# Optimization experiments

Measured on AMD Instinct MI355X. Metric: run time of the kernel, lower is better.

Reference implementation:

```python
import jax, jax.numpy as jnp
import numpy as np

N, C, H, W = 128, 3, 256, 256
MAXNORM = 5.371920351148152
MAX_SQ = 16  # static bound for data-dependent squaring loop
PADE_B = [6.476475253248e+16, 3.238237626624e+16, 7771770303897600.0,
          1187353796428800.0, 129060195264000.0, 10559470521600.0,
          670442572800.0, 33522128640.0, 1323241920.0, 40840800.0,
          960960.0, 16380.0, 182.0, 1.0]


def pade13(A):
    b = PADE_B
    I = jnp.eye(A.shape[-1], dtype=A.dtype)
    A2 = A @ A
    A4 = A2 @ A2
    A6 = A4 @ A2
    U = A @ (A6 @ (b[13] * A6 + b[11] * A4 + b[9] * A2)
             + b[7] * A6 + b[5] * A4 + b[3] * A2 + b[1] * I)
    V = (A6 @ (b[12] * A6 + b[10] * A4 + b[8] * A2)
         + b[6] * A6 + b[4] * A4 + b[2] * A2 + b[0] * I)
    return U, V


def expm_affine(theta):  # theta: [N,2,3] -> exp of padded 3x3, top 2 rows
    n = theta.shape[0]
    A = jnp.concatenate([theta, jnp.zeros((n, 1, 3), theta.dtype)], axis=1)
    fro = jnp.sqrt(jnp.sum(A * A, axis=(1, 2), keepdims=True))
    n_sq = jnp.maximum(0.0, jnp.ceil(jnp.log2(fro / MAXNORM)))
    Asc = A / (2.0 ** n_sq)
    U, V = pade13(Asc)
    R = jnp.linalg.solve(U + V, -U + V)
    k = n_sq.reshape(n).astype(jnp.int32)
    def body(i, Rc):
        return jnp.where((i < k)[:, None, None], jnp.matmul(Rc, Rc), Rc)
    R = jax.lax.fori_loop(0, MAX_SQ, body, R)
    return R[:, :2, :]


def affine_grid(theta, Ho, Wo):  # align_corners=True
    xs = jnp.linspace(-1.0, 1.0, Wo, dtype=theta.dtype)
    ys = jnp.linspace(-1.0, 1.0, Ho, dtype=theta.dtype)
    gy, gx = jnp.meshgrid(ys, xs, indexing='ij')          # [Ho,Wo]
    base = jnp.stack([gx, gy, jnp.ones_like(gx)], axis=-1)  # [Ho,Wo,3]
    return jnp.einsum('hwk,nck->nhwc', base, theta)        # [N,Ho,Wo,2]


def grid_sample(x, grid):  # bilinear, zeros padding, align_corners=True
    _, _, Hi, Wi = x.shape
    ix = (grid[..., 0] + 1.0) * 0.5 * (Wi - 1)
    iy = (grid[..., 1] + 1.0) * 0.5 * (Hi - 1)
    ix0 = jnp.floor(ix)
    iy0 = jnp.floor(iy)
    ix1 = ix0 + 1.0
    iy1 = iy0 + 1.0
    wx1 = ix - ix0; wx0 = 1.0 - wx1
    wy1 = iy - iy0; wy0 = 1.0 - wy1

    def gather(yy, xx):
        valid = ((yy >= 0) & (yy < Hi) & (xx >= 0) & (xx < Wi))
        yc = jnp.clip(yy, 0, Hi - 1).astype(jnp.int32)
        xc = jnp.clip(xx, 0, Wi - 1).astype(jnp.int32)
        vals = jax.vmap(lambda img, y, xi: img[:, y, xi])(x, yc, xc)  # [N,C,Ho,Wo]
        return vals * valid[:, None].astype(x.dtype)

    return (gather(iy0, ix0) * (wy0 * wx0)[:, None]
            + gather(iy0, ix1) * (wy0 * wx1)[:, None]
            + gather(iy1, ix0) * (wy1 * wx0)[:, None]
            + gather(iy1, ix1) * (wy1 * wx1)[:, None])


def setup_inputs() -> dict:
    key = jax.random.key(0)
    k1, k2 = jax.random.split(key)
    x = jax.random.normal(k1, (N, C, H, W), dtype=jnp.float32)
    theta = 0.1 * jax.random.normal(k2, (N, 6), dtype=jnp.float32)
    return {"x": x, "theta": theta}


def reference(x, theta):
    th = expm_affine(theta.reshape(-1, 2, 3))  # [N,2,3]
    grid = affine_grid(th, H, W)               # [N,H,W,2]
    return grid_sample(x, grid)                # [N,C,H,W]
```

## Files before the change

### kernel.cpp

```cpp
#include <hip/hip_runtime.h>

#define Ndim 128
#define Cdim 3
#define Hdim 256
#define Wdim 256
#define HW (Hdim * Wdim)
#define MAXNORM_F 5.371920351148152f

#define LCOLS 56
#define LROWS 48
#define LBUF  (LCOLS * LROWS)

typedef float vf2 __attribute__((ext_vector_type(2)));
typedef unsigned int uint32;

__device__ __forceinline__ void mm3f(const float a[3][3], const float b[3][3], float c[3][3]) {
    #pragma unroll
    for (int i = 0; i < 3; ++i)
        #pragma unroll
        for (int j = 0; j < 3; ++j) {
            float s = 0.0f;
            #pragma unroll
            for (int k = 0; k < 3; ++k) s = fmaf(a[i][k], b[k][j], s);
            c[i][j] = s;
        }
}

__global__ void expm_kernel(const float* __restrict__ theta, float* __restrict__ thOut) {
    int n = blockIdx.x * blockDim.x + threadIdx.x;
    if (n >= Ndim) return;

    const float b[14] = {6.476475253248e+16f, 3.238237626624e+16f, 7771770303897600.0f,
                         1187353796428800.0f, 129060195264000.0f, 10559470521600.0f,
                         670442572800.0f, 33522128640.0f, 1323241920.0f, 40840800.0f,
                         960960.0f, 16380.0f, 182.0f, 1.0f};

    float A[3][3];
    #pragma unroll
    for (int j = 0; j < 3; ++j) {
        A[0][j] = theta[n * 6 + j];
        A[1][j] = theta[n * 6 + 3 + j];
        A[2][j] = 0.0f;
    }

    float fro2 = 0.0f;
    #pragma unroll
    for (int i = 0; i < 3; ++i)
        #pragma unroll
        for (int j = 0; j < 3; ++j) fro2 = fmaf(A[i][j], A[i][j], fro2);
    float fro = sqrtf(fro2);

    float nsq = fmaxf(0.0f, ceilf(log2f(fro / MAXNORM_F)));
    int k = (int)nsq;
    float sc = exp2f(-nsq);
    #pragma unroll
    for (int i = 0; i < 3; ++i)
        #pragma unroll
        for (int j = 0; j < 3; ++j) A[i][j] *= sc;

    float A2[3][3], A4[3][3], A6[3][3], P[3][3], Wm[3][3], T[3][3], U[3][3], V[3][3];
    mm3f(A, A, A2);
    mm3f(A2, A2, A4);
    mm3f(A4, A2, A6);

    #pragma unroll
    for (int i = 0; i < 3; ++i)
        #pragma unroll
        for (int j = 0; j < 3; ++j)
            P[i][j] = b[13] * A6[i][j] + b[11] * A4[i][j] + b[9] * A2[i][j];
    mm3f(A6, P, T);
    #pragma unroll
    for (int i = 0; i < 3; ++i)
        #pragma unroll
        for (int j = 0; j < 3; ++j)
            Wm[i][j] = T[i][j] + b[7] * A6[i][j] + b[5] * A4[i][j] + b[3] * A2[i][j]
                       + (i == j ? b[1] : 0.0f);
    mm3f(A, Wm, U);

    #pragma unroll
    for (int i = 0; i < 3; ++i)
        #pragma unroll
        for (int j = 0; j < 3; ++j)
            P[i][j] = b[12] * A6[i][j] + b[10] * A4[i][j] + b[8] * A2[i][j];
    mm3f(A6, P, T);
    #pragma unroll
    for (int i = 0; i < 3; ++i)
        #pragma unroll
        for (int j = 0; j < 3; ++j)
            V[i][j] = T[i][j] + b[6] * A6[i][j] + b[4] * A4[i][j] + b[2] * A2[i][j]
                      + (i == j ? b[0] : 0.0f);

    float M[3][6];
    #pragma unroll
    for (int i = 0; i < 3; ++i)
        #pragma unroll
        for (int j = 0; j < 3; ++j) {
            M[i][j]     = U[i][j] + V[i][j];
            M[i][j + 3] = V[i][j] - U[i][j];
        }
    #pragma unroll
    for (int col = 0; col < 3; ++col) {
        int piv = col;
        float best = fabsf(M[col][col]);
        for (int r = col + 1; r < 3; ++r) {
            float v = fabsf(M[r][col]);
            if (v > best) { best = v; piv = r; }
        }
        if (piv != col) {
            #pragma unroll
            for (int j = 0; j < 6; ++j) {
                float t = M[col][j]; M[col][j] = M[piv][j]; M[piv][j] = t;
            }
        }
        float inv = 1.0f / M[col][col];
        #pragma unroll
        for (int j = 0; j < 6; ++j) M[col][j] *= inv;
        #pragma unroll
        for (int r = 0; r < 3; ++r) {
            if (r == col) continue;
            float f = M[r][col];
            #pragma unroll
            for (int j = 0; j < 6; ++j) M[r][j] -= f * M[col][j];
        }
    }
    float R[3][3];
    #pragma unroll
    for (int i = 0; i < 3; ++i)
        #pragma unroll
        for (int j = 0; j < 3; ++j) R[i][j] = M[i][j + 3];

    for (int i = 0; i < 16; ++i) {
        if (i < k) {
            float Rn[3][3];
            mm3f(R, R, Rn);
            #pragma unroll
            for (int a = 0; a < 3; ++a)
                #pragma unroll
                for (int c = 0; c < 3; ++c) R[a][c] = Rn[a][c];
        }
    }

    #pragma unroll
    for (int j = 0; j < 3; ++j) {
        thOut[n * 6 + j]     = (float)R[0][j];
        thOut[n * 6 + 3 + j] = (float)R[1][j];
    }
}

__global__ __launch_bounds__(256) void sample_kernel(const float* __restrict__ x,
                                                     const float* __restrict__ th,
                                                     float* __restrict__ out) {
    __shared__ float lds[2][LBUF];

    const int nwg_per_xcd = 8192 / 8;
    int bid = blockIdx.x;
    int wgid = (bid & 7) * nwg_per_xcd + (bid >> 3);

    int tw  = wgid & 7;
    int thp = (wgid >> 3) & 7;
    int n   = wgid >> 6;

    int tid = threadIdx.x;
    int w  = (tw << 5) + (tid & 31);
    int h0 = (thp << 5) + ((tid >> 5) << 2);

    const float* t = th + n * 6;
    float t0 = t[0], t1 = t[1], t2 = t[2], t3 = t[3], t4 = t[4], t5 = t[5];

    float Cx = 127.5f * (t2 - t0 - t1 + 1.0f);
    float Cy = 127.5f * (t5 - t3 - t4 + 1.0f);

    float fwA = (float)(tw << 5),  fwB = fwA + 31.0f;
    float fhA = (float)(thp << 5), fhB = fhA + 31.0f;
    float xlo = fminf(fwA * t0, fwB * t0) + fminf(fhA * t1, fhB * t1) + Cx;
    float xhi = fmaxf(fwA * t0, fwB * t0) + fmaxf(fhA * t1, fhB * t1) + Cx;
    float ylo = fminf(fwA * t3, fwB * t3) + fminf(fhA * t4, fhB * t4) + Cy;
    float yhi = fmaxf(fwA * t3, fwB * t3) + fmaxf(fhA * t4, fhB * t4) + Cy;
    int Xlo = (int)floorf(xlo) - 1, Xhi = (int)floorf(xhi) + 2;
    int Ylo = (int)floorf(ylo) - 1, Yhi = (int)floorf(yhi) + 2;
    int cn = Xhi - Xlo + 1;
    int rn = Yhi - Ylo + 1;

    size_t nbase = (size_t)n * Cdim * HW;

    float ixs[4], iys[4];
    float ixb = fmaf((float)w, t0, fmaf((float)h0, t1, Cx));
    float iyb = fmaf((float)w, t3, fmaf((float)h0, t4, Cy));
    #pragma unroll
    for (int p = 0; p < 4; ++p) {
        ixs[p] = fmaf((float)p, t1, ixb);
        iys[p] = fmaf((float)p, t4, iyb);
    }

    bool fast = (cn <= 52) && (rn <= LROWS) && (rn >= 1) && (cn >= 1);

    if (fast) {
        int bxw = (min(max(Xlo, 0), Wdim - LCOLS)) & ~3;
        int byw = min(max(Ylo, 0), Hdim - rn);
        int totc = 14 * rn;
        const float* gbase = x + nbase;

        auto stage = [&](int ch, int buf) {
            #pragma unroll
            for (int it = 0; it < 3; ++it) {
                int k = (it << 8) + tid;
                if (k < totc) {
                    int row = k / 14;
                    int col = k - row * 14;
                    const float* gp = gbase + (size_t)ch * HW
                                    + ((byw + row) << 8) + bxw + (col << 2);
                    __builtin_amdgcn_global_load_lds(
                        (const __attribute__((address_space(1))) uint32*)gp,
                        (__attribute__((address_space(3))) uint32*)
                            ((uint32*)&lds[buf][0] + ((size_t)k << 2)),
                        16, 0, 0);
                }
            }
        };

        bool interior = (Xlo >= 0) && (Xhi <= Wdim - 1) && (Ylo >= 0) && (Yhi <= Hdim - 1);

        stage(0, 0);

        int   basev[4];
        float wx1v[4], wx0v[4], wy1v[4], wy0v[4];
        if (interior) {
            #pragma unroll
            for (int p = 0; p < 4; ++p) {
                float ix = ixs[p], iy = iys[p];
                float fx = floorf(ix), fy = floorf(iy);
                wx1v[p] = ix - fx; wx0v[p] = 1.0f - wx1v[p];
                wy1v[p] = iy - fy; wy0v[p] = 1.0f - wy1v[p];
                basev[p] = ((int)fy - byw) * LCOLS + ((int)fx - bxw);
            }
        }
        size_t p0 = (size_t)h0 * Wdim + w;

        auto sample_interior = [&](int buf, int c) {
            float* o = out + nbase + (size_t)c * HW + p0;
            #pragma unroll
            for (int p = 0; p < 4; ++p) {
                const float* bp = &lds[buf][basev[p]];
                float v00 = bp[0],     v01 = bp[1];
                float v10 = bp[LCOLS], v11 = bp[LCOLS + 1];
                float top = fmaf(v01, wx1v[p], v00 * wx0v[p]);
                float bot = fmaf(v11, wx1v[p], v10 * wx0v[p]);
                o[(size_t)p * Wdim] = fmaf(wy1v[p], bot, wy0v[p] * top);
            }
        };

        auto sample_edge = [&](int buf, int c) {
            float* o = out + nbase + (size_t)c * HW + p0;
            #pragma unroll
            for (int p = 0; p < 4; ++p) {
                float ix = ixs[p], iy = iys[p];
                float fx = floorf(ix), fy = floorf(iy);
                int x0i = (int)fx, y0i = (int)fy;
                float wx1 = ix - fx, wx0 = 1.0f - wx1;
                float wy1 = iy - fy, wy0 = 1.0f - wy1;
                float mx0 = ((unsigned)x0i       < (unsigned)Wdim) ? 1.0f : 0.0f;
                float mx1 = ((unsigned)(x0i + 1) < (unsigned)Wdim) ? 1.0f : 0.0f;
                float my0 = ((unsigned)y0i       < (unsigned)Hdim) ? 1.0f : 0.0f;
                float my1 = ((unsigned)(y0i + 1) < (unsigned)Hdim) ? 1.0f : 0.0f;
                float wxm0 = wx0 * mx0, wxm1 = wx1 * mx1;
                float wym0 = wy0 * my0, wym1 = wy1 * my1;

                int lx0 = min(max(x0i - bxw, 0), LCOLS - 1);
                int lx1 = min(max(x0i + 1 - bxw, 0), LCOLS - 1);
                int ly0 = min(max(y0i - byw, 0), rn - 1);
                int ly1 = min(max(y0i + 1 - byw, 0), rn - 1);
                const float* B = &lds[buf][0];
                float v00 = B[ly0 * LCOLS + lx0], v01 = B[ly0 * LCOLS + lx1];
                float v10 = B[ly1 * LCOLS + lx0], v11 = B[ly1 * LCOLS + lx1];
                float top = fmaf(v01, wxm1, v00 * wxm0);
                float bot = fmaf(v11, wxm1, v10 * wxm0);
                o[(size_t)p * Wdim] = fmaf(wym1, bot, wym0 * top);
            }
        };

        __syncthreads();
        stage(1, 1);
        if (interior) sample_interior(0, 0); else sample_edge(0, 0);
        __syncthreads();
        stage(2, 0);
        if (interior) sample_interior(1, 1); else sample_edge(1, 1);
        __syncthreads();
        if (interior) sample_interior(0, 2); else sample_edge(0, 2);
    } else {
        const float* img0 = x + nbase;
        #pragma unroll
        for (int p = 0; p < 4; ++p) {
            float ix = ixs[p], iy = iys[p];
            float fx = floorf(ix), fy = floorf(iy);
            int ix0 = (int)fx, iy0 = (int)fy;
            float wx1 = ix - fx, wx0 = 1.0f - wx1;
            float wy1 = iy - fy, wy0 = 1.0f - wy1;
            float mx0 = ((unsigned)ix0       < (unsigned)Wdim) ? 1.0f : 0.0f;
            float mx1 = ((unsigned)(ix0 + 1) < (unsigned)Wdim) ? 1.0f : 0.0f;
            float my0 = ((unsigned)iy0       < (unsigned)Hdim) ? 1.0f : 0.0f;
            float my1 = ((unsigned)(iy0 + 1) < (unsigned)Hdim) ? 1.0f : 0.0f;
            int xc0 = min(max(ix0, 0), Wdim - 1);
            int xc1 = min(max(ix0 + 1, 0), Wdim - 1);
            int yc0 = min(max(iy0, 0), Hdim - 1);
            int yc1 = min(max(iy0 + 1, 0), Hdim - 1);
            float w00 = wy0 * wx0 * my0 * mx0;
            float w01 = wy0 * wx1 * my0 * mx1;
            float w10 = wy1 * wx0 * my1 * mx0;
            float w11 = wy1 * wx1 * my1 * mx1;
            int o00 = yc0 * Wdim + xc0, o01 = yc0 * Wdim + xc1;
            int o10 = yc1 * Wdim + xc0, o11 = yc1 * Wdim + xc1;
            #pragma unroll
            for (int c = 0; c < Cdim; ++c) {
                const float* img = img0 + (size_t)c * HW;
                float r = fmaf(img[o00], w00, fmaf(img[o01], w01,
                          fmaf(img[o10], w10, img[o11] * w11)));
                out[nbase + (size_t)c * HW + (size_t)(h0 + p) * Wdim + w] = r;
            }
        }
    }
}

extern "C" void kernel_launch(void* const* d_in, const int* in_sizes, int n_in,
                              void* d_out, int out_size, void* d_ws, size_t ws_size,
                              hipStream_t stream) {
    const float* x     = (const float*)d_in[0];
    const float* theta = (const float*)d_in[1];
    float* out = (float*)d_out;
    float* th  = (float*)d_ws;

    expm_kernel<<<1, 128, 0, stream>>>(theta, th);

    sample_kernel<<<8192, 256, 0, stream>>>(x, th, out);
}
```

Before: 42.01 us.

## Process four row tiles per workgroup with continuous cross-tile LDS double buffering

Each workgroup now handles four vertically adjacent 32x32 tiles instead of one, and the grid shrinks from 8192 to 2048 blocks. The LDS staging pipeline runs across tiles, so channel 0 of the next tile is prefetched while channel 2 of the current tile is sampled. This removes the per-workgroup prologue with its unhidden first load and cuts launch and scheduling overhead. In exchange there are fewer blocks in flight, more register pressure, and the fast path is taken only when all four tiles qualify.

```diff
diff --git a/kernel.cpp b/kernel.cpp
--- a/kernel.cpp
+++ b/kernel.cpp
@@ -11,7 +11,6 @@
 #define LROWS 48
 #define LBUF  (LCOLS * LROWS)
 
-typedef float vf2 __attribute__((ext_vector_type(2)));
 typedef unsigned int uint32;
 
 __device__ __forceinline__ void mm3f(const float a[3][3], const float b[3][3], float c[3][3]) {
@@ -147,22 +146,39 @@
     }
 }
 
+__device__ __forceinline__ void stage_ch(const float* __restrict__ gch, int bxw, int byw,
+                                         int rn, float* __restrict__ buf, int tid) {
+    int totc = 14 * rn;
+    #pragma unroll
+    for (int it = 0; it < 3; ++it) {
+        int k = (it << 8) + tid;
+        if (k < totc) {
+            int row = k / 14;
+            int col = k - row * 14;
+            const float* gp = gch + ((byw + row) << 8) + bxw + (col << 2);
+            __builtin_amdgcn_global_load_lds(
+                (const __attribute__((address_space(1))) uint32*)gp,
+                (__attribute__((address_space(3))) uint32*)((uint32*)buf + ((size_t)k << 2)),
+                16, 0, 0);
+        }
+    }
+}
+
 __global__ __launch_bounds__(256) void sample_kernel(const float* __restrict__ x,
                                                      const float* __restrict__ th,
                                                      float* __restrict__ out) {
     __shared__ float lds[2][LBUF];
 
-    const int nwg_per_xcd = 8192 / 8;
+    const int nwg_per_xcd = 2048 / 8;
     int bid = blockIdx.x;
     int wgid = (bid & 7) * nwg_per_xcd + (bid >> 3);
 
     int tw  = wgid & 7;
-    int thp = (wgid >> 3) & 7;
-    int n   = wgid >> 6;
+    int thg = (wgid >> 3) & 1;
+    int n   = wgid >> 4;
 
     int tid = threadIdx.x;
-    int w  = (tw << 5) + (tid & 31);
-    int h0 = (thp << 5) + ((tid >> 5) << 2);
+    int w = (tw << 5) + (tid & 31);
 
     const float* t = th + n * 6;
     float t0 = t[0], t1 = t[1], t2 = t[2], t3 = t[3], t4 = t[4], t5 = t[5];
@@ -170,151 +186,161 @@
     float Cx = 127.5f * (t2 - t0 - t1 + 1.0f);
     float Cy = 127.5f * (t5 - t3 - t4 + 1.0f);
 
-    float fwA = (float)(tw << 5),  fwB = fwA + 31.0f;
-    float fhA = (float)(thp << 5), fhB = fhA + 31.0f;
-    float xlo = fminf(fwA * t0, fwB * t0) + fminf(fhA * t1, fhB * t1) + Cx;
-    float xhi = fmaxf(fwA * t0, fwB * t0) + fmaxf(fhA * t1, fhB * t1) + Cx;
-    float ylo = fminf(fwA * t3, fwB * t3) + fminf(fhA * t4, fhB * t4) + Cy;
-    float yhi = fmaxf(fwA * t3, fwB * t3) + fmaxf(fhA * t4, fhB * t4) + Cy;
-    int Xlo = (int)floorf(xlo) - 1, Xhi = (int)floorf(xhi) + 2;
-    int Ylo = (int)floorf(ylo) - 1, Yhi = (int)floorf(yhi) + 2;
-    int cn = Xhi - Xlo + 1;
-    int rn = Yhi - Ylo + 1;
+    float fwA = (float)(tw << 5), fwB = fwA + 31.0f;
+
+    int bxws[4], byws[4], rns[4];
+    bool inters[4], fasts[4];
+    bool fastAll = true;
+    #pragma unroll
+    for (int tt = 0; tt < 4; ++tt) {
+        int thp = (thg << 2) + tt;
+        float fhA = (float)(thp << 5), fhB = fhA + 31.0f;
+        float xlo = fminf(fwA * t0, fwB * t0) + fminf(fhA * t1, fhB * t1) + Cx;
+        float xhi = fmaxf(fwA * t0, fwB * t0) + fmaxf(fhA * t1, fhB * t1) + Cx;
+        float ylo = fminf(fwA * t3, fwB * t3) + fminf(fhA * t4, fhB * t4) + Cy;
+        float yhi = fmaxf(fwA * t3, fwB * t3) + fmaxf(fhA * t4, fhB * t4) + Cy;
+        int Xlo = (int)floorf(xlo) - 1, Xhi = (int)floorf(xhi) + 2;
+        int Ylo = (int)floorf(ylo) - 1, Yhi = (int)floorf(yhi) + 2;
+        int cn = Xhi - Xlo + 1;
+        int rn = Yhi - Ylo + 1;
+        rn = min(max(rn, 1), 200);
+        bool f = (cn <= 52) && (cn >= 1) && (rn <= LROWS);
+        fasts[tt] = f;
+        fastAll &= f;
+        bxws[tt] = (min(max(Xlo, 0), Wdim - LCOLS)) & ~3;
+        byws[tt] = min(max(Ylo, 0), Hdim - rn);
+        rns[tt]  = rn;
+        inters[tt] = (Xlo >= 0) && (Xhi <= Wdim - 1) && (Ylo >= 0) && (Yhi <= Hdim - 1);
+    }
 
     size_t nbase = (size_t)n * Cdim * HW;
-
-    float ixs[4], iys[4];
-    float ixb = fmaf((float)w, t0, fmaf((float)h0, t1, Cx));
-    float iyb = fmaf((float)w, t3, fmaf((float)h0, t4, Cy));
-    #pragma unroll
-    for (int p = 0; p < 4; ++p) {
-        ixs[p] = fmaf((float)p, t1, ixb);
-        iys[p] = fmaf((float)p, t4, iyb);
-    }
-
-    bool fast = (cn <= 52) && (rn <= LROWS) && (rn >= 1) && (cn >= 1);
-
-    if (fast) {
-        int bxw = (min(max(Xlo, 0), Wdim - LCOLS)) & ~3;
-        int byw = min(max(Ylo, 0), Hdim - rn);
-        int totc = 14 * rn;
-        const float* gbase = x + nbase;
-
-        auto stage = [&](int ch, int buf) {
-            #pragma unroll
-            for (int it = 0; it < 3; ++it) {
-                int k = (it << 8) + tid;
-                if (k < totc) {
-                    int row = k / 14;
-                    int col = k - row * 14;
-                    const float* gp = gbase + (size_t)ch * HW
-                                    + ((byw + row) << 8) + bxw + (col << 2);
-                    __builtin_amdgcn_global_load_lds(
-                        (const __attribute__((address_space(1))) uint32*)gp,
-                        (__attribute__((address_space(3))) uint32*)
-                            ((uint32*)&lds[buf][0] + ((size_t)k << 2)),
-                        16, 0, 0);
+    const float* gbase = x + nbase;
+
+    if (fastAll) {
+        stage_ch(gbase, bxws[0], byws[0], rns[0], lds[0], tid);
+
+        #pragma unroll
+        for (int tt = 0; tt < 4; ++tt) {
+            int thp = (thg << 2) + tt;
+            int h0 = (thp << 5) + ((tid >> 5) << 2);
+            int bxw = bxws[tt], byw = byws[tt], rn = rns[tt];
+            bool inter = inters[tt];
+
+            float ixs[4], iys[4];
+            float ixb = fmaf((float)w, t0, fmaf((float)h0, t1, Cx));
+            float iyb = fmaf((float)w, t3, fmaf((float)h0, t4, Cy));
+            #pragma unroll
+            for (int p = 0; p < 4; ++p) {
+                ixs[p] = fmaf((float)p, t1, ixb);
+                iys[p] = fmaf((float)p, t4, iyb);
+            }
+
+            int   basev[4];
+            float wx1v[4], wx0v[4], wy1v[4], wy0v[4];
+            if (inter) {
+                #pragma unroll
+                for (int p = 0; p < 4; ++p) {
+                    float fx = floorf(ixs[p]), fy = floorf(iys[p]);
+                    wx1v[p] = ixs[p] - fx; wx0v[p] = 1.0f - wx1v[p];
+                    wy1v[p] = iys[p] - fy; wy0v[p] = 1.0f - wy1v[p];
+                    basev[p] = ((int)fy - byw) * LCOLS + ((int)fx - bxw);
                 }
             }
-        };
-
-        bool interior = (Xlo >= 0) && (Xhi <= Wdim - 1) && (Ylo >= 0) && (Yhi <= Hdim - 1);
-
-        stage(0, 0);
-
-        int   basev[4];
-        float wx1v[4], wx0v[4], wy1v[4], wy0v[4];
-        if (interior) {
+            size_t p0 = (size_t)h0 * Wdim + w;
+
+            auto sampleI = [&](int buf, int c) {
+                float* o = out + nbase + (size_t)c * HW + p0;
+                #pragma unroll
+                for (int p = 0; p < 4; ++p) {
+                    const float* bp = &lds[buf][basev[p]];
+                    float v00 = bp[0],     v01 = bp[1];
+                    float v10 = bp[LCOLS], v11 = bp[LCOLS + 1];
+                    float top = fmaf(v01, wx1v[p], v00 * wx0v[p]);
+                    float bot = fmaf(v11, wx1v[p], v10 * wx0v[p]);
+                    o[(size_t)p * Wdim] = fmaf(wy1v[p], bot, wy0v[p] * top);
+                }
+            };
+            auto sampleE = [&](int buf, int c) {
+                float* o = out + nbase + (size_t)c * HW + p0;
+                #pragma unroll
+                for (int p = 0; p < 4; ++p) {
+                    float ix = ixs[p], iy = iys[p];
+                    float fx = floorf(ix), fy = floorf(iy);
+                    int x0i = (int)fx, y0i = (int)fy;
+                    float wx1 = ix - fx, wx0 = 1.0f - wx1;
+                    float wy1 = iy - fy, wy0 = 1.0f - wy1;
+                    float mx0 = ((unsigned)x0i       < (unsigned)Wdim) ? 1.0f : 0.0f;
+                    float mx1 = ((unsigned)(x0i + 1) < (unsigned)Wdim) ? 1.0f : 0.0f;
+                    float my0 = ((unsigned)y0i       < (unsigned)Hdim) ? 1.0f : 0.0f;
+                    float my1 = ((unsigned)(y0i + 1) < (unsigned)Hdim) ? 1.0f : 0.0f;
+                    float wxm0 = wx0 * mx0, wxm1 = wx1 * mx1;
+                    float wym0 = wy0 * my0, wym1 = wy1 * my1;
+                    int lx0 = min(max(x0i - bxw, 0), LCOLS - 1);
+                    int lx1 = min(max(x0i + 1 - bxw, 0), LCOLS - 1);
+                    int ly0 = min(max(y0i - byw, 0), rn - 1);
+                    int ly1 = min(max(y0i + 1 - byw, 0), rn - 1);
+                    const float* B = &lds[buf][0];
+                    float v00 = B[ly0 * LCOLS + lx0], v01 = B[ly0 * LCOLS + lx1];
+                    float v10 = B[ly1 * LCOLS + lx0], v11 = B[ly1 * LCOLS + lx1];
+                    float top = fmaf(v01, wxm1, v00 * wxm0);
+                    float bot = fmaf(v11, wxm1, v10 * wxm0);
+                    o[(size_t)p * Wdim] = fmaf(wym1, bot, wym0 * top);
+                }
+            };
+
+            const int bA = tt & 1, bB = bA ^ 1;
+            __syncthreads();
+            stage_ch(gbase + HW, bxw, byw, rn, lds[bB], tid);
+            if (inter) sampleI(bA, 0); else sampleE(bA, 0);
+            __syncthreads();
+            stage_ch(gbase + 2 * HW, bxw, byw, rn, lds[bA], tid);
+            if (inter) sampleI(bB, 1); else sampleE(bB, 1);
+            __syncthreads();
+            if (tt < 3)
+                stage_ch(gbase, bxws[tt + 1], byws[tt + 1], rns[tt + 1], lds[bB], tid);
+            if (inter) sampleI(bA, 2); else sampleE(bA, 2);
+        }
+    } else {
+        for (int tt = 0; tt < 4; ++tt) {
+            int thp = (thg << 2) + tt;
+            int h0 = (thp << 5) + ((tid >> 5) << 2);
+
+            float ixs[4], iys[4];
+            float ixb = fmaf((float)w, t0, fmaf((float)h0, t1, Cx));
+            float iyb = fmaf((float)w, t3, fmaf((float)h0, t4, Cy));
+            #pragma unroll
+            for (int p = 0; p < 4; ++p) {
+                ixs[p] = fmaf((float)p, t1, ixb);
+                iys[p] = fmaf((float)p, t4, iyb);
+            }
             #pragma unroll
             for (int p = 0; p < 4; ++p) {
                 float ix = ixs[p], iy = iys[p];
                 float fx = floorf(ix), fy = floorf(iy);
-                wx1v[p] = ix - fx; wx0v[p] = 1.0f - wx1v[p];
-                wy1v[p] = iy - fy; wy0v[p] = 1.0f - wy1v[p];
-                basev[p] = ((int)fy - byw) * LCOLS + ((int)fx - bxw);
-            }
-        }
-        size_t p0 = (size_t)h0 * Wdim + w;
-
-        auto sample_interior = [&](int buf, int c) {
-            float* o = out + nbase + (size_t)c * HW + p0;
-            #pragma unroll
-            for (int p = 0; p < 4; ++p) {
-                const float* bp = &lds[buf][basev[p]];
-                float v00 = bp[0],     v01 = bp[1];
-                float v10 = bp[LCOLS], v11 = bp[LCOLS + 1];
-                float top = fmaf(v01, wx1v[p], v00 * wx0v[p]);
-                float bot = fmaf(v11, wx1v[p], v10 * wx0v[p]);
-                o[(size_t)p * Wdim] = fmaf(wy1v[p], bot, wy0v[p] * top);
-            }
-        };
-
-        auto sample_edge = [&](int buf, int c) {
-            float* o = out + nbase + (size_t)c * HW + p0;
-            #pragma unroll
-            for (int p = 0; p < 4; ++p) {
-                float ix = ixs[p], iy = iys[p];
-                float fx = floorf(ix), fy = floorf(iy);
-                int x0i = (int)fx, y0i = (int)fy;
+                int ix0 = (int)fx, iy0 = (int)fy;
                 float wx1 = ix - fx, wx0 = 1.0f - wx1;
                 float wy1 = iy - fy, wy0 = 1.0f - wy1;
-                float mx0 = ((unsigned)x0i       < (unsigned)Wdim) ? 1.0f : 0.0f;
-                float mx1 = ((unsigned)(x0i + 1) < (unsigned)Wdim) ? 1.0f : 0.0f;
-                float my0 = ((unsigned)y0i       < (unsigned)Hdim) ? 1.0f : 0.0f;
-                float my1 = ((unsigned)(y0i + 1) < (unsigned)Hdim) ? 1.0f : 0.0f;
-                float wxm0 = wx0 * mx0, wxm1 = wx1 * mx1;
-                float wym0 = wy0 * my0, wym1 = wy1 * my1;
-
-                int lx0 = min(max(x0i - bxw, 0), LCOLS - 1);
-                int lx1 = min(max(x0i + 1 - bxw, 0), LCOLS - 1);
-                int ly0 = min(max(y0i - byw, 0), rn - 1);
-                int ly1 = min(max(y0i + 1 - byw, 0), rn - 1);
-                const float* B = &lds[buf][0];
-                float v00 = B[ly0 * LCOLS + lx0], v01 = B[ly0 * LCOLS + lx1];
-                float v10 = B[ly1 * LCOLS + lx0], v11 = B[ly1 * LCOLS + lx1];
-                float top = fmaf(v01, wxm1, v00 * wxm0);
-                float bot = fmaf(v11, wxm1, v10 * wxm0);
-                o[(size_t)p * Wdim] = fmaf(wym1, bot, wym0 * top);
-            }
-        };
-
-        __syncthreads();
-        stage(1, 1);
-        if (interior) sample_interior(0, 0); else sample_edge(0, 0);
-        __syncthreads();
-        stage(2, 0);
-        if (interior) sample_interior(1, 1); else sample_edge(1, 1);
-        __syncthreads();
-        if (interior) sample_interior(0, 2); else sample_edge(0, 2);
-    } else {
-        const float* img0 = x + nbase;
-        #pragma unroll
-        for (int p = 0; p < 4; ++p) {
-            float ix = ixs[p], iy = iys[p];
-            float fx = floorf(ix), fy = floorf(iy);
-            int ix0 = (int)fx, iy0 = (int)fy;
-            float wx1 = ix - fx, wx0 = 1.0f - wx1;
-            float wy1 = iy - fy, wy0 = 1.0f - wy1;
-            float mx0 = ((unsigned)ix0       < (unsigned)Wdim) ? 1.0f : 0.0f;
-            float mx1 = ((unsigned)(ix0 + 1) < (unsigned)Wdim) ? 1.0f : 0.0f;
-            float my0 = ((unsigned)iy0       < (unsigned)Hdim) ? 1.0f : 0.0f;
-            float my1 = ((unsigned)(iy0 + 1) < (unsigned)Hdim) ? 1.0f : 0.0f;
-            int xc0 = min(max(ix0, 0), Wdim - 1);
-            int xc1 = min(max(ix0 + 1, 0), Wdim - 1);
-            int yc0 = min(max(iy0, 0), Hdim - 1);
-            int yc1 = min(max(iy0 + 1, 0), Hdim - 1);
-            float w00 = wy0 * wx0 * my0 * mx0;
-            float w01 = wy0 * wx1 * my0 * mx1;
-            float w10 = wy1 * wx0 * my1 * mx0;
-            float w11 = wy1 * wx1 * my1 * mx1;
-            int o00 = yc0 * Wdim + xc0, o01 = yc0 * Wdim + xc1;
-            int o10 = yc1 * Wdim + xc0, o11 = yc1 * Wdim + xc1;
-            #pragma unroll
-            for (int c = 0; c < Cdim; ++c) {
-                const float* img = img0 + (size_t)c * HW;
-                float r = fmaf(img[o00], w00, fmaf(img[o01], w01,
-                          fmaf(img[o10], w10, img[o11] * w11)));
-                out[nbase + (size_t)c * HW + (size_t)(h0 + p) * Wdim + w] = r;
+                float mx0 = ((unsigned)ix0       < (unsigned)Wdim) ? 1.0f : 0.0f;
+                float mx1 = ((unsigned)(ix0 + 1) < (unsigned)Wdim) ? 1.0f : 0.0f;
+                float my0 = ((unsigned)iy0       < (unsigned)Hdim) ? 1.0f : 0.0f;
+                float my1 = ((unsigned)(iy0 + 1) < (unsigned)Hdim) ? 1.0f : 0.0f;
+                int xc0 = min(max(ix0, 0), Wdim - 1);
+                int xc1 = min(max(ix0 + 1, 0), Wdim - 1);
+                int yc0 = min(max(iy0, 0), Hdim - 1);
+                int yc1 = min(max(iy0 + 1, 0), Hdim - 1);
+                float w00 = wy0 * wx0 * my0 * mx0;
+                float w01 = wy0 * wx1 * my0 * mx1;
+                float w10 = wy1 * wx0 * my1 * mx0;
+                float w11 = wy1 * wx1 * my1 * mx1;
+                int o00 = yc0 * Wdim + xc0, o01 = yc0 * Wdim + xc1;
+                int o10 = yc1 * Wdim + xc0, o11 = yc1 * Wdim + xc1;
+                #pragma unroll
+                for (int c = 0; c < Cdim; ++c) {
+                    const float* img = gbase + (size_t)c * HW;
+                    float r = fmaf(img[o00], w00, fmaf(img[o01], w01,
+                              fmaf(img[o10], w10, img[o11] * w11)));
+                    out[nbase + (size_t)c * HW + (size_t)(h0 + p) * Wdim + w] = r;
+                }
             }
         }
     }
@@ -330,5 +356,5 @@
 
     expm_kernel<<<1, 128, 0, stream>>>(theta, th);
 
-    sample_kernel<<<8192, 256, 0, stream>>>(x, th, out);
-}
+    sample_kernel<<<2048, 256, 0, stream>>>(x, th, out);
+}
```

After: 50.04 us. 1.19x slower.
